# Kernel tuning notes

Measured on AMD Instinct MI355X. Metric: run time of the kernel, lower is better.

## Reference

```python
import jax, jax.numpy as jnp
import numpy as np

NUM_CODES = 1024
CODE_DIM = 256
COMMIT_W = 0.25
EPS = 1e-5
ENT_LO, ENT_HI = 0.5, 0.9
ENT_W = 0.1
VAR_FLOOR = 0.05
VAR_W = 1e-3
DECORR_W = 1e-3


def setup_inputs() -> dict:
    key = jax.random.key(0)
    k1, k2, k3 = jax.random.split(key, 3)
    inputs = jax.random.normal(k1, (16, 2048, CODE_DIM), dtype=jnp.float32)
    weight = jax.random.normal(k2, (NUM_CODES, CODE_DIM), dtype=jnp.float32) * 0.1
    usage_counts = jax.random.uniform(k3, (NUM_CODES,), dtype=jnp.float32)
    return {"inputs": inputs, "weight": weight, "usage_counts": usage_counts}


def reference(inputs, weight, usage_counts):
    K, D = weight.shape
    flat = inputs.reshape(-1, D)  # [N, D]
    # squared euclidean distances [N, K]
    dist = (flat ** 2).sum(axis=1, keepdims=True) - 2.0 * flat @ weight.T + (weight ** 2).sum(axis=1)
    idx = jnp.argmin(dist, axis=1)  # [N]
    quant = weight[idx].reshape(inputs.shape)

    commitment_loss = COMMIT_W * jnp.mean((jax.lax.stop_gradient(quant) - inputs) ** 2)
    # straight-through estimator
    quant_ste = inputs + jax.lax.stop_gradient(quant - inputs)

    # usage entropy regularizer
    probs = usage_counts + EPS
    probs = probs / jnp.maximum(probs.sum(), EPS * K)
    usage_entropy = -jnp.sum(probs * jnp.log(probs + EPS)) / np.log(float(K)).astype(np.float32)
    gap = jnp.where(usage_entropy < ENT_LO, ENT_LO - usage_entropy,
                    jnp.where(usage_entropy > ENT_HI, usage_entropy - ENT_HI, 0.0))
    entropy_loss = ENT_W * gap ** 2

    # variance floor penalty on codebook
    variance = jnp.var(weight, axis=0)
    variance_loss = VAR_W * jnp.mean(jax.nn.relu(VAR_FLOOR - variance))

    # decorrelation penalty
    wc = weight - weight.mean(axis=0, keepdims=True)
    cov = wc.T @ wc / float(K)  # [D, D]
    off_diag = cov - jnp.diag(jnp.diag(cov))
    decorrelation_loss = DECORR_W * jnp.mean(off_diag ** 2)

    total_loss = commitment_loss + entropy_loss + variance_loss + decorrelation_loss
    indices = idx.reshape(inputs.shape[:-1])
    return (quant_ste, indices, total_loss, commitment_loss, entropy_loss,
            variance_loss, decorrelation_loss, usage_entropy)
```

## Files before the change

### kernel.cpp

```cpp
#include <hip/hip_runtime.h>
#include <math.h>

#define DIMS   256
#define KCODES 1024
#define NTOT   32768
#define TAU    4.0e-4f

typedef __bf16 bf16x8 __attribute__((ext_vector_type(8)));
typedef float  f32x4  __attribute__((ext_vector_type(4)));

#define WS_COMMIT   0
#define WS_FLAGCNT  1
#define WS_DECORR   2
#define WS_COLSUM   16
#define WS_COLSQ    272
#define WS_WSQ      1024
#define WS_XSQ      2048
#define WS_FLAGS    34816
#define WS_CAND1    67584
#define WS_CAND2    329728
#define WS_CANDI    591872
#define WS_WP       854016

#define OUT_Q    0
#define OUT_IDX  8388608
#define OUT_SCAL 8421376


__global__ __launch_bounds__(256) void prep_kernel(const float* __restrict__ X,
                                                   const float* __restrict__ W,
                                                   __bf16* __restrict__ Xp,
                                                   __bf16* __restrict__ Wp2,
                                                   float* ws) {
  int b = blockIdx.x;
  int tid = threadIdx.x;
  if (b < 1056) {
    bool isW = b >= 1024;
    const float* src = isW ? W : X;
    __bf16* dst = isW ? Wp2 : Xp;
    int sqoff = isW ? WS_WSQ : WS_XSQ;
    int bb = isW ? b - 1024 : b;
    int kt = tid >> 5, mtl = (tid >> 4) & 1, lc = tid & 15;
    int row = bb * 32 + mtl * 16 + lc;
    int bt = row >> 7, c = row & 127;
    int wv = c >> 6, t = (c >> 4) & 3;
    size_t hibase = ((((size_t)(bt * 8 + kt) * 2 + wv) * 4 + t) * 2) * 512;
    const float* s = src + (size_t)row * DIMS + kt * 32;
    float sq = 0.f;
    #pragma unroll
    for (int kq = 0; kq < 4; kq++) {
      float4 u = *(const float4*)(s + kq * 8);
      float4 v = *(const float4*)(s + kq * 8 + 4);
      float f[8] = {u.x, u.y, u.z, u.w, v.x, v.y, v.z, v.w};
      bf16x8 hi, lo;
      #pragma unroll
      for (int e = 0; e < 8; e++) {
        __bf16 h = (__bf16)f[e];
        hi[e] = h;
        lo[e] = (__bf16)(f[e] - (float)h);
        sq = fmaf(f[e], f[e], sq);
      }
      size_t off = (size_t)(kq * 16 + lc) * 8;
      *(bf16x8*)&dst[hibase + off] = hi;
      *(bf16x8*)&dst[hibase + 512 + off] = lo;
    }
    atomicAdd(&ws[sqoff + row], sq);
  } else if (b < 1064) {
    int d = tid;
    int r0 = (b - 1056) * 128;
    float s = 0.f, sq = 0.f;
    #pragma unroll 8
    for (int k = 0; k < 128; k++) {
      float v = W[(size_t)(r0 + k) * DIMS + d];
      s += v;
      sq = fmaf(v, v, sq);
    }
    atomicAdd(&ws[WS_COLSUM + d], s);
    atomicAdd(&ws[WS_COLSQ + d], sq);
  } else {
    __shared__ float wi_s[2][KCODES];
    __shared__ float red2[256];
    __shared__ float mi_s[2];
    __shared__ float red[4];
    int i0 = (b - 1064) * 2;
    int rr = tid >> 1, cc = tid & 1;
    #pragma unroll
    for (int q = 0; q < 8; q++) {
      int row = q * 128 + rr;
      wi_s[cc][row] = W[(size_t)row * DIMS + i0 + cc];
    }
    __syncthreads();
    float pm = 0.f;
    #pragma unroll
    for (int q = 0; q < 8; q++) pm += wi_s[cc][rr * 8 + q];
    red2[tid] = pm;
    __syncthreads();
    if (tid < 2) {
      float s = 0.f;
      for (int k = tid; k < 256; k += 2) s += red2[k];
      mi_s[tid] = s * (1.0f / 1024.0f);
    }
    int j = tid;
    float a0 = 0.f, a1 = 0.f, sj = 0.f;
    for (int k = 0; k < KCODES; k += 4) {
      #pragma unroll
      for (int u = 0; u < 4; u++) {
        float wj = W[(size_t)(k + u) * DIMS + j];
        a0 = fmaf(wi_s[0][k + u], wj, a0);
        a1 = fmaf(wi_s[1][k + u], wj, a1);
        sj += wj;
      }
    }
    __syncthreads();
    const float inv = 1.0f / 1024.0f;
    float mj = sj * inv;
    float v = 0.f;
    float c0 = a0 * inv - mi_s[0] * mj;
    if (i0 != j) v = fmaf(c0, c0, v);
    float c1 = a1 * inv - mi_s[1] * mj;
    if (i0 + 1 != j) v = fmaf(c1, c1, v);
    #pragma unroll
    for (int m = 32; m >= 1; m >>= 1) v += __shfl_xor(v, m);
    if ((j & 63) == 0) red[j >> 6] = v;
    __syncthreads();
    if (j == 0) atomicAdd(&ws[WS_DECORR], (red[0] + red[1]) + (red[2] + red[3]));
  }
}

__global__ __launch_bounds__(256, 2) void pass1_kernel(const __bf16* __restrict__ Xp,
                                                       const __bf16* __restrict__ Wp2,
                                                       float* ws) {
  __shared__ float wsqs[128];
  __shared__ float d1L[256];
  __shared__ float d2L[256];
  __shared__ int   i1L[256];

  int tid = threadIdx.x;
  int lane = tid & 63, wave = tid >> 6;
  int wm = wave >> 1, wn = wave & 1;
  int quad = lane >> 4, col = lane & 15;
  int l = blockIdx.x;
  int bm = (l & 7) * 32 + ((l >> 3) & 31);
  int bn = l >> 8;
  int rowBase = bm * 128, cb = bn * 128;

  if (tid < 128) wsqs[tid] = ws[WS_WSQ + cb + tid];

  f32x4 acc[4][4];
  #pragma unroll
  for (int i = 0; i < 4; i++)
    #pragma unroll
    for (int j = 0; j < 4; j++) acc[i][j] = (f32x4){0.f, 0.f, 0.f, 0.f};

  const bf16x8* ab = (const bf16x8*)(Xp + (size_t)bm * 65536 + wm * 4096) + lane;
  const bf16x8* bb = (const bf16x8*)(Wp2 + (size_t)bn * 65536 + wn * 4096) + lane;

  bf16x8 Af[2][8], Bf[2][8];
  #pragma unroll
  for (int f = 0; f < 4; f++) {
    Af[0][f * 2] = ab[f * 128];
    Af[0][f * 2 + 1] = ab[f * 128 + 64];
    Bf[0][f * 2] = bb[f * 128];
    Bf[0][f * 2 + 1] = bb[f * 128 + 64];
  }
  #pragma unroll
  for (int kt = 0; kt < 8; kt++) {
    const int cur = kt & 1, nxt = cur ^ 1;
    if (kt < 7) {
      const bf16x8* an = ab + (kt + 1) * 1024;
      const bf16x8* bv = bb + (kt + 1) * 1024;
      #pragma unroll
      for (int f = 0; f < 4; f++) {
        Af[nxt][f * 2] = an[f * 128];
        Af[nxt][f * 2 + 1] = an[f * 128 + 64];
        Bf[nxt][f * 2] = bv[f * 128];
        Bf[nxt][f * 2 + 1] = bv[f * 128 + 64];
      }
    }
    #pragma unroll
    for (int nt = 0; nt < 4; nt++) {
      #pragma unroll
      for (int mt = 0; mt < 4; mt++) {
        acc[mt][nt] = __builtin_amdgcn_mfma_f32_16x16x32_bf16(Af[cur][mt * 2], Bf[cur][nt * 2], acc[mt][nt], 0, 0, 0);
        acc[mt][nt] = __builtin_amdgcn_mfma_f32_16x16x32_bf16(Af[cur][mt * 2], Bf[cur][nt * 2 + 1], acc[mt][nt], 0, 0, 0);
        acc[mt][nt] = __builtin_amdgcn_mfma_f32_16x16x32_bf16(Af[cur][mt * 2 + 1], Bf[cur][nt * 2], acc[mt][nt], 0, 0, 0);
      }
    }
  }
  __syncthreads();

  #pragma unroll
  for (int mt = 0; mt < 4; mt++) {
    #pragma unroll
    for (int r = 0; r < 4; r++) {
      float d1 = 3.0e38f, d2 = 3.0e38f;
      int i1 = 0;
      #pragma unroll
      for (int nt = 0; nt < 4; nt++) {
        int lc = wn * 64 + nt * 16 + col;
        float d = wsqs[lc] - 2.0f * acc[mt][nt][r];
        int g = cb + lc;
        if (d < d1) { d2 = d1; d1 = d; i1 = g; }
        else if (d < d2) d2 = d;
      }
      #pragma unroll
      for (int m = 1; m < 16; m <<= 1) {
        float od1 = __shfl_xor(d1, m);
        int oi1 = __shfl_xor(i1, m);
        float od2 = __shfl_xor(d2, m);
        if (od1 < d1 || (od1 == d1 && oi1 < i1)) {
          d2 = fminf(d1, fminf(d2, od2));
          d1 = od1; i1 = oi1;
        } else {
          d2 = fminf(od1, fminf(d2, od2));
        }
      }
      if (col == 0) {
        int lr = wm * 64 + mt * 16 + quad * 4 + r;
        d1L[lr * 2 + wn] = d1;
        d2L[lr * 2 + wn] = d2;
        i1L[lr * 2 + wn] = i1;
      }
    }
  }
  __syncthreads();
  if (tid < 128) {
    float a1 = d1L[tid * 2], a2 = d2L[tid * 2];
    int ai = i1L[tid * 2];
    float b1 = d1L[tid * 2 + 1], b2 = d2L[tid * 2 + 1];
    int bi = i1L[tid * 2 + 1];
    float m1, m2; int mi;
    if (b1 < a1 || (b1 == a1 && bi < ai)) { m1 = b1; mi = bi; m2 = fminf(a1, b2); }
    else { m1 = a1; mi = ai; m2 = fminf(b1, a2); }
    int o = bn * NTOT + rowBase + tid;
    ws[WS_CAND1 + o] = m1;
    ws[WS_CAND2 + o] = m2;
    ((int*)ws)[WS_CANDI + o] = mi;
  }
}

__global__ __launch_bounds__(256) void pass2_kernel(const float* __restrict__ W,
                                                    float* __restrict__ outQ,
                                                    float* __restrict__ outIdx, float* ws) {
  __shared__ int idx_s[256];
  int tid = threadIdx.x;
  int row = blockIdx.x * 256 + tid;
  const float* c1 = ws + WS_CAND1;
  const float* c2 = ws + WS_CAND2;
  const int* ci = (const int*)ws + WS_CANDI;
  float m1 = 3.0e38f, m2 = 3.0e38f;
  int mi = 0;
  #pragma unroll
  for (int b = 0; b < 8; b++) {
    int o = b * NTOT + row;
    float b1 = c1[o], b2 = c2[o];
    int bi = ci[o];
    if (b1 < m1 || (b1 == m1 && bi < mi)) { m2 = fminf(m1, b2); m1 = b1; mi = bi; }
    else { m2 = fminf(m2, b1); }
  }
  outIdx[row] = (float)mi;
  idx_s[tid] = mi;
  int* wsI = (int*)ws;
  if (m2 - m1 < TAU) {
    int p = atomicAdd(&wsI[WS_FLAGCNT], 1);
    wsI[WS_FLAGS + p] = row;
  }
  float partial = ws[WS_XSQ + row] + m1;
  #pragma unroll
  for (int m = 32; m >= 1; m >>= 1) partial += __shfl_xor(partial, m);
  if ((tid & 63) == 0) atomicAdd(&ws[WS_COMMIT], partial);
  __syncthreads();
  int wave = tid >> 6, lane = tid & 63;
  int rowBase = blockIdx.x * 256;
  #pragma unroll 4
  for (int i = 0; i < 64; i++) {
    int rl = wave * 64 + i;
    int ix = idx_s[rl];
    float4 v = ((const float4*)(W + (size_t)ix * DIMS))[lane];
    ((float4*)(outQ + (size_t)(rowBase + rl) * DIMS))[lane] = v;
  }
}

__global__ __launch_bounds__(256) void refine_kernel(const float* __restrict__ X,
                                                     const float* __restrict__ W,
                                                     float* __restrict__ outQ,
                                                     float* __restrict__ outIdx, float* ws,
                                                     const float* __restrict__ U,
                                                     float* __restrict__ out) {
  __shared__ float xs[DIMS];
  __shared__ double dm[256];
  __shared__ int im[256];
  __shared__ int chosen;
  int tid = threadIdx.x;
  if (blockIdx.x == 512) {
    __shared__ float red[256];
    float s = 0.f;
    for (int e = tid; e < KCODES; e += 256) s += U[e] + 1e-5f;
    red[tid] = s;
    __syncthreads();
    for (int st = 128; st >= 1; st >>= 1) {
      if (tid < st) red[tid] += red[tid + st];
      __syncthreads();
    }
    float S = red[0];
    __syncthreads();
    float denom = fmaxf(S, 1e-5f * 1024.0f);
    float h = 0.f;
    for (int e = tid; e < KCODES; e += 256) {
      float p = (U[e] + 1e-5f) / denom;
      h += p * logf(p + 1e-5f);
    }
    red[tid] = h;
    __syncthreads();
    for (int st = 128; st >= 1; st >>= 1) {
      if (tid < st) red[tid] += red[tid + st];
      __syncthreads();
    }
    float H = -red[0] / 6.93147180559945f;
    __syncthreads();
    float m = ws[WS_COLSUM + tid] * (1.0f / 1024.0f);
    float var = ws[WS_COLSQ + tid] * (1.0f / 1024.0f) - m * m;
    float r = 0.05f - var;
    red[tid] = r > 0.f ? r : 0.f;
    __syncthreads();
    for (int st = 128; st >= 1; st >>= 1) {
      if (tid < st) red[tid] += red[tid + st];
      __syncthreads();
    }
    if (tid == 0) {
      float varloss = 1e-3f * (red[0] / 256.0f);
      float gap = H < 0.5f ? (0.5f - H) : (H > 0.9f ? (H - 0.9f) : 0.0f);
      float entloss = 0.1f * gap * gap;
      float commit = 0.25f * ws[WS_COMMIT] / 8388608.0f;
      float dec = 1e-3f * ws[WS_DECORR] / 65536.0f;
      float* sc = out + OUT_SCAL;
      sc[0] = commit + entloss + varloss + dec;
      sc[1] = commit;
      sc[2] = entloss;
      sc[3] = varloss;
      sc[4] = dec;
      sc[5] = H;
    }
    return;
  }
  const int* wsI = (const int*)ws;
  int cnt = wsI[WS_FLAGCNT];
  const int* list = wsI + WS_FLAGS;
  for (int f = blockIdx.x; f < cnt; f += 512) {
    int row = list[f];
    __syncthreads();
    if (tid < 64) ((float4*)xs)[tid] = ((const float4*)(X + (size_t)row * DIMS))[tid];
    __syncthreads();
    double bd = 1.0e300;
    int bi = 0;
    for (int jj = 0; jj < 4; jj++) {
      int c = tid + 256 * jj;
      double a0 = 0.0, a1 = 0.0, a2 = 0.0, a3 = 0.0;
      const float* wr = W + (size_t)c * DIMS;
      #pragma unroll 4
      for (int d4 = 0; d4 < 64; d4++) {
        float4 w = ((const float4*)wr)[d4];
        float4 x = ((const float4*)xs)[d4];
        double e0 = (double)x.x - (double)w.x;
        double e1 = (double)x.y - (double)w.y;
        double e2 = (double)x.z - (double)w.z;
        double e3 = (double)x.w - (double)w.w;
        a0 += e0 * e0; a1 += e1 * e1; a2 += e2 * e2; a3 += e3 * e3;
      }
      double s = (a0 + a1) + (a2 + a3);
      if (s < bd) { bd = s; bi = c; }
    }
    dm[tid] = bd; im[tid] = bi;
    __syncthreads();
    for (int st = 128; st >= 1; st >>= 1) {
      if (tid < st) {
        if (dm[tid + st] < dm[tid] || (dm[tid + st] == dm[tid] && im[tid + st] < im[tid])) {
          dm[tid] = dm[tid + st]; im[tid] = im[tid + st];
        }
      }
      __syncthreads();
    }
    if (tid == 0) { chosen = im[0]; outIdx[row] = (float)im[0]; }
    __syncthreads();
    int ix = chosen;
    if (tid < 64)
      ((float4*)(outQ + (size_t)row * DIMS))[tid] = ((const float4*)(W + (size_t)ix * DIMS))[tid];
  }
}

extern "C" void kernel_launch(void* const* d_in, const int* in_sizes, int n_in, void* d_out,
                              int out_size, void* d_ws, size_t ws_size, hipStream_t stream) {
  const float* X = (const float*)d_in[0];
  const float* W = (const float*)d_in[1];
  const float* U = (const float*)d_in[2];
  float* out = (float*)d_out;
  float* ws = (float*)d_ws;
  __bf16* Xp = (__bf16*)(out + OUT_Q);
  __bf16* Wp2 = (__bf16*)(ws + WS_WP);

  hipMemsetAsync(d_ws, 0, 139264, stream);
  prep_kernel<<<1192, 256, 0, stream>>>(X, W, Xp, Wp2, ws);
  pass1_kernel<<<2048, 256, 0, stream>>>(Xp, Wp2, ws);
  pass2_kernel<<<NTOT / 256, 256, 0, stream>>>(W, out + OUT_Q, out + OUT_IDX, ws);
  refine_kernel<<<513, 256, 0, stream>>>(X, W, out + OUT_Q, out + OUT_IDX, ws, U, out);
}
```

Measured before the change: 236.7 us.

## Stage pass1 GEMM tiles through LDS with triple-buffered async global-to-LDS loads

Pass1 now uses 512-thread blocks on a 256x128 tile. X and codebook slices are staged into a three-slot LDS ring via global_load_lds, with explicit vmcnt waits and barriers, where before each wave loaded its fragments straight from global memory into registers. Blocks are remapped with a new swizzle and MFMA sections run at raised wave priority. The goal is to share loads across waves, raise operand reuse and hide memory latency behind MFMA work. The cost is a large LDS footprint (about 144KB per block), which limits occupancy, plus many barriers per k-step.

```diff
diff --git a/kernel.cpp b/kernel.cpp
--- a/kernel.cpp
+++ b/kernel.cpp
@@ -127,24 +127,43 @@
   }
 }
 
-__global__ __launch_bounds__(256, 2) void pass1_kernel(const __bf16* __restrict__ Xp,
+__device__ __forceinline__ void stage16(const __bf16* g, __bf16* l) {
+  __builtin_amdgcn_global_load_lds(
+      (const __attribute__((address_space(1))) void*)g,
+      (__attribute__((address_space(3))) void*)l, 16, 0, 0);
+}
+
+#define STAGE_PIECE(T, J) do {                                                    \
+    int _s = (T) % 3;                                                             \
+    if ((J) < 4) {                                                                \
+      int _c = (J) >> 1, _h = (J) & 1;                                            \
+      stage16(Xp + (size_t)((2 * bm + _c) * 8 + (T)) * 8192 + _h * 4096 + tid * 8,\
+              buf + _s * 24576 + _c * 8192 + _h * 4096 + tid * 8);                \
+    } else {                                                                      \
+      int _h = (J) - 4;                                                           \
+      stage16(Wp2 + (size_t)(bn * 8 + (T)) * 8192 + _h * 4096 + tid * 8,          \
+              buf + _s * 24576 + 16384 + _h * 4096 + tid * 8);                    \
+    }                                                                             \
+  } while (0)
+
+__global__ __launch_bounds__(512, 2) void pass1_kernel(const __bf16* __restrict__ Xp,
                                                        const __bf16* __restrict__ Wp2,
                                                        float* ws) {
+  __shared__ __align__(16) __bf16 buf[73728];
   __shared__ float wsqs[128];
-  __shared__ float d1L[256];
-  __shared__ float d2L[256];
-  __shared__ int   i1L[256];
+  __shared__ float d1L[512];
+  __shared__ float d2L[512];
+  __shared__ int   i1L[512];
 
   int tid = threadIdx.x;
   int lane = tid & 63, wave = tid >> 6;
   int wm = wave >> 1, wn = wave & 1;
   int quad = lane >> 4, col = lane & 15;
   int l = blockIdx.x;
-  int bm = (l & 7) * 32 + ((l >> 3) & 31);
-  int bn = l >> 8;
-  int rowBase = bm * 128, cb = bn * 128;
-
-  if (tid < 128) wsqs[tid] = ws[WS_WSQ + cb + tid];
+  int swz = (l & 7) * 128 + (l >> 3);
+  int bm = swz >> 3;
+  int bn = swz & 7;
+  int cb = bn * 128;
 
   f32x4 acc[4][4];
   #pragma unroll
@@ -152,42 +171,56 @@
     #pragma unroll
     for (int j = 0; j < 4; j++) acc[i][j] = (f32x4){0.f, 0.f, 0.f, 0.f};
 
-  const bf16x8* ab = (const bf16x8*)(Xp + (size_t)bm * 65536 + wm * 4096) + lane;
-  const bf16x8* bb = (const bf16x8*)(Wp2 + (size_t)bn * 65536 + wn * 4096) + lane;
-
-  bf16x8 Af[2][8], Bf[2][8];
-  #pragma unroll
-  for (int f = 0; f < 4; f++) {
-    Af[0][f * 2] = ab[f * 128];
-    Af[0][f * 2 + 1] = ab[f * 128 + 64];
-    Bf[0][f * 2] = bb[f * 128];
-    Bf[0][f * 2 + 1] = bb[f * 128 + 64];
-  }
+  wsqs[tid & 127] = ws[WS_WSQ + cb + (tid & 127)];
+  asm volatile("" ::: "memory");
+
+  #pragma unroll
+  for (int t = 0; t < 3; t++) {
+    STAGE_PIECE(t, 0); STAGE_PIECE(t, 1); STAGE_PIECE(t, 2);
+    STAGE_PIECE(t, 3); STAGE_PIECE(t, 4); STAGE_PIECE(t, 5);
+  }
+  asm volatile("s_waitcnt vmcnt(12)" ::: "memory");
+  __builtin_amdgcn_s_barrier();
+
   #pragma unroll
   for (int kt = 0; kt < 8; kt++) {
-    const int cur = kt & 1, nxt = cur ^ 1;
-    if (kt < 7) {
-      const bf16x8* an = ab + (kt + 1) * 1024;
-      const bf16x8* bv = bb + (kt + 1) * 1024;
+    const __bf16* bsl = buf + (kt % 3) * 24576 + lane * 8;
+    bf16x8 Bf[4][2];
+    #pragma unroll
+    for (int p = 0; p < 4; p++) {
+      bf16x8 A0 = *(const bf16x8*)(bsl + wm * 4096 + (p * 2 + 0) * 512);
+      bf16x8 A1 = *(const bf16x8*)(bsl + wm * 4096 + (p * 2 + 1) * 512);
+      if (p == 0) {
+        #pragma unroll
+        for (int nt = 0; nt < 4; nt++) {
+          Bf[nt][0] = *(const bf16x8*)(bsl + 16384 + wn * 4096 + (nt * 2 + 0) * 512);
+          Bf[nt][1] = *(const bf16x8*)(bsl + 16384 + wn * 4096 + (nt * 2 + 1) * 512);
+        }
+      }
+      if (kt + 2 < 8) {
+        if (p == 0) { STAGE_PIECE(kt + 2, 0); STAGE_PIECE(kt + 2, 1); }
+        if (p == 1) { STAGE_PIECE(kt + 2, 2); STAGE_PIECE(kt + 2, 3); }
+        if (p == 2) { STAGE_PIECE(kt + 2, 4); }
+        if (p == 3) { STAGE_PIECE(kt + 2, 5); }
+      }
+      if (p == 3 && kt < 7) {
+        if (kt <= 5) asm volatile("s_waitcnt vmcnt(6)" ::: "memory");
+        else         asm volatile("s_waitcnt vmcnt(0)" ::: "memory");
+      }
+      __builtin_amdgcn_s_barrier();
+      asm volatile("s_waitcnt lgkmcnt(0)" ::: "memory");
+      __builtin_amdgcn_sched_barrier(0);
+      __builtin_amdgcn_s_setprio(1);
       #pragma unroll
-      for (int f = 0; f < 4; f++) {
-        Af[nxt][f * 2] = an[f * 128];
-        Af[nxt][f * 2 + 1] = an[f * 128 + 64];
-        Bf[nxt][f * 2] = bv[f * 128];
-        Bf[nxt][f * 2 + 1] = bv[f * 128 + 64];
-      }
-    }
-    #pragma unroll
-    for (int nt = 0; nt < 4; nt++) {
-      #pragma unroll
-      for (int mt = 0; mt < 4; mt++) {
-        acc[mt][nt] = __builtin_amdgcn_mfma_f32_16x16x32_bf16(Af[cur][mt * 2], Bf[cur][nt * 2], acc[mt][nt], 0, 0, 0);
-        acc[mt][nt] = __builtin_amdgcn_mfma_f32_16x16x32_bf16(Af[cur][mt * 2], Bf[cur][nt * 2 + 1], acc[mt][nt], 0, 0, 0);
-        acc[mt][nt] = __builtin_amdgcn_mfma_f32_16x16x32_bf16(Af[cur][mt * 2 + 1], Bf[cur][nt * 2], acc[mt][nt], 0, 0, 0);
-      }
-    }
-  }
-  __syncthreads();
+      for (int nt = 0; nt < 4; nt++) {
+        acc[p][nt] = __builtin_amdgcn_mfma_f32_16x16x32_bf16(A0, Bf[nt][0], acc[p][nt], 0, 0, 0);
+        acc[p][nt] = __builtin_amdgcn_mfma_f32_16x16x32_bf16(A0, Bf[nt][1], acc[p][nt], 0, 0, 0);
+        acc[p][nt] = __builtin_amdgcn_mfma_f32_16x16x32_bf16(A1, Bf[nt][0], acc[p][nt], 0, 0, 0);
+      }
+      __builtin_amdgcn_s_setprio(0);
+      __builtin_amdgcn_s_barrier();
+    }
+  }
 
   #pragma unroll
   for (int mt = 0; mt < 4; mt++) {
@@ -224,7 +257,7 @@
     }
   }
   __syncthreads();
-  if (tid < 128) {
+  if (tid < 256) {
     float a1 = d1L[tid * 2], a2 = d2L[tid * 2];
     int ai = i1L[tid * 2];
     float b1 = d1L[tid * 2 + 1], b2 = d2L[tid * 2 + 1];
@@ -232,7 +265,7 @@
     float m1, m2; int mi;
     if (b1 < a1 || (b1 == a1 && bi < ai)) { m1 = b1; mi = bi; m2 = fminf(a1, b2); }
     else { m1 = a1; mi = ai; m2 = fminf(b1, a2); }
-    int o = bn * NTOT + rowBase + tid;
+    int o = bn * NTOT + bm * 256 + tid;
     ws[WS_CAND1 + o] = m1;
     ws[WS_CAND2 + o] = m2;
     ((int*)ws)[WS_CANDI + o] = mi;
@@ -400,7 +433,7 @@
 
   hipMemsetAsync(d_ws, 0, 139264, stream);
   prep_kernel<<<1192, 256, 0, stream>>>(X, W, Xp, Wp2, ws);
-  pass1_kernel<<<2048, 256, 0, stream>>>(Xp, Wp2, ws);
+  pass1_kernel<<<1024, 512, 0, stream>>>(Xp, Wp2, ws);
   pass2_kernel<<<NTOT / 256, 256, 0, stream>>>(W, out + OUT_Q, out + OUT_IDX, ws);
   refine_kernel<<<513, 256, 0, stream>>>(X, W, out + OUT_Q, out + OUT_IDX, ws, U, out);
 }
```

Result: slower. 254.0 us (+7.3%).
